# Optimization experiments

Measured on AMD Instinct MI355X. Metric: run time of the kernel, lower is better.

The kernel has to match this reference:

```python
import jax, jax.numpy as jnp
import numpy as np

B, TQ, TK, E, H, DH = 4, 1024, 1024, 1024, 16, 64
EPS = 1e-5

def setup_inputs() -> dict:
    key = jax.random.key(0)
    ks = jax.random.split(key, 16)
    s = 0.02
    return {
        "x": jax.random.normal(ks[0], (B, TQ, E), jnp.float32),
        "encoder_out": jax.random.normal(ks[1], (B, TK, E), jnp.float32),
        "Q1w": jax.random.normal(ks[2], (H, DH, E), jnp.float32) * s,
        "Q1b": jax.random.normal(ks[3], (H, DH), jnp.float32) * s,
        "Q2w": jax.random.normal(ks[4], (H, DH, E), jnp.float32) * s,
        "Q2b": jax.random.normal(ks[5], (H, DH), jnp.float32) * s,
        "K1w": jax.random.normal(ks[6], (H, DH, E), jnp.float32) * s,
        "K1b": jax.random.normal(ks[7], (H, DH), jnp.float32) * s,
        "K2w": jax.random.normal(ks[8], (H, DH, E), jnp.float32) * s,
        "K2b": jax.random.normal(ks[9], (H, DH), jnp.float32) * s,
        "Vw": jax.random.normal(ks[10], (H, DH, E), jnp.float32) * s,
        "Vb": jax.random.normal(ks[11], (H, DH), jnp.float32) * s,
        "lam": jax.random.uniform(ks[12], (H,), jnp.float32, 0.5, 1.0),
        "gn_gamma": jnp.ones((H * DH,), jnp.float32),
        "gn_beta": jnp.zeros((H * DH,), jnp.float32),
        "out_w": jax.random.normal(ks[13], (E, H * DH), jnp.float32) * s,
        "out_b": jax.random.normal(ks[14], (E,), jnp.float32) * s,
    }

def _proj(inp, w, b):
    # inp: [B,T,E], w: [H,DH,E] -> [B,H,T,DH]
    return jnp.einsum('bte,hde->bhtd', inp, w) + b[None, :, None, :]

def reference(x, encoder_out, Q1w, Q1b, Q2w, Q2b, K1w, K1b, K2w, K2b, Vw, Vb,
              lam, gn_gamma, gn_beta, out_w, out_b):
    scale = 1.0 / jnp.sqrt(jnp.float32(DH))
    q1 = _proj(x, Q1w, Q1b)
    q2 = _proj(x, Q2w, Q2b)
    k1 = _proj(encoder_out, K1w, K1b)
    k2 = _proj(encoder_out, K2w, K2b)
    v = _proj(encoder_out, Vw, Vb)
    s1 = jnp.einsum('bhtd,bhsd->bhts', q1, k1) * scale  # [B,H,TQ,TK]
    s2 = jnp.einsum('bhtd,bhsd->bhts', q2, k2) * scale
    w = jax.nn.softmax(s1, axis=-1) - lam[None, :, None, None] * jax.nn.softmax(s2, axis=-1)
    out = jnp.einsum('bhts,bhsd->bhtd', w, v)  # [B,H,TQ,DH]
    # GroupNorm(num_groups=H, channels=H*DH) over [B,C,T]: per (B,H) stats over (T,DH)
    mu = jnp.mean(out, axis=(2, 3), keepdims=True)
    var = jnp.mean(jnp.square(out - mu), axis=(2, 3), keepdims=True)
    normed = (out - mu) * jax.lax.rsqrt(var + EPS)
    g = gn_gamma.reshape(H, DH)[None, :, None, :]
    b_ = gn_beta.reshape(H, DH)[None, :, None, :]
    normed = normed * g + b_
    y = normed.transpose(0, 2, 1, 3).reshape(B, TQ, H * DH)
    return y @ out_w.T + out_b
```

## Files before the change

kernel.cpp:

```cpp
#include <hip/hip_runtime.h>
#include <cmath>

typedef __bf16 bf16_t;
typedef bf16_t bf16x8 __attribute__((ext_vector_type(8)));
typedef bf16_t bf16x4 __attribute__((ext_vector_type(4)));
typedef float  f32x4  __attribute__((ext_vector_type(4)));

#define Bn  4
#define TQn 1024
#define TKn 1024
#define En  1024
#define Hn  16
#define DHn 64

static constexpr float EPSv = 1e-5f;
static constexpr float C_SCALE = 0.18033688011112042f;

#define GLDS16(g, l)                                                         \
    __builtin_amdgcn_global_load_lds(                                        \
        (const __attribute__((address_space(1))) void*)(g),                  \
        (__attribute__((address_space(3))) void*)(l), 16, 0, 0)

__global__ __launch_bounds__(256)
void cvt_all(const float* __restrict__ x, const float* __restrict__ enc,
             const float* __restrict__ q1w, const float* __restrict__ q2w,
             const float* __restrict__ k1w, const float* __restrict__ k2w,
             const float* __restrict__ vw,  const float* __restrict__ outw,
             bf16_t* __restrict__ xb, bf16_t* __restrict__ encb,
             bf16_t* __restrict__ wq, bf16_t* __restrict__ wkv,
             bf16_t* __restrict__ wob)
{
    int idx = blockIdx.x * 256 + threadIdx.x;
    const float* src; bf16_t* dst;
    if      (idx < 1048576) { src = x    + (size_t)idx * 4;              dst = xb   + (size_t)idx * 4; }
    else if (idx < 2097152) { src = enc  + (size_t)(idx - 1048576) * 4;  dst = encb + (size_t)(idx - 1048576) * 4; }
    else if (idx < 2359296) { src = q1w  + (size_t)(idx - 2097152) * 4;  dst = wq   + (size_t)(idx - 2097152) * 4; }
    else if (idx < 2621440) { src = q2w  + (size_t)(idx - 2359296) * 4;  dst = wq   + 1048576 + (size_t)(idx - 2359296) * 4; }
    else if (idx < 2883584) { src = k1w  + (size_t)(idx - 2621440) * 4;  dst = wkv  + (size_t)(idx - 2621440) * 4; }
    else if (idx < 3145728) { src = k2w  + (size_t)(idx - 2883584) * 4;  dst = wkv  + 1048576 + (size_t)(idx - 2883584) * 4; }
    else if (idx < 3407872) { src = vw   + (size_t)(idx - 3145728) * 4;  dst = wkv  + 2097152 + (size_t)(idx - 3145728) * 4; }
    else                    { src = outw + (size_t)(idx - 3407872) * 4;  dst = wob  + (size_t)(idx - 3407872) * 4; }
    float4 v = *(const float4*)src;
    bf16x4 o;
    o[0] = (bf16_t)v.x; o[1] = (bf16_t)v.y; o[2] = (bf16_t)v.z; o[3] = (bf16_t)v.w;
    *(bf16x4*)dst = o;
}

__global__ __launch_bounds__(256, 3)
void gemm_proj(const bf16_t* __restrict__ xb, const bf16_t* __restrict__ encb,
               const bf16_t* __restrict__ wq, const bf16_t* __restrict__ wkv,
               const float* __restrict__ q1b, const float* __restrict__ q2b,
               const float* __restrict__ k1b, const float* __restrict__ k2b,
               const float* __restrict__ vb,
               bf16_t* __restrict__ q12, bf16_t* __restrict__ k12v)
{
    __shared__ bf16_t sA[128 * 64];
    __shared__ bf16_t sB[128 * 64];
    int bx = blockIdx.x;
    const bf16_t* A; const bf16_t* W; bf16_t* C; const float* bp; int blockN;
    if (bx < 16) {
        A = xb; W = wq; C = q12; blockN = bx << 7;
        bp = (blockN >> 10) ? q2b : q1b;
    } else {
        bx -= 16;
        A = encb; W = wkv; C = k12v; blockN = bx << 7;
        const int seg = blockN >> 10;
        bp = (seg == 0) ? k1b : ((seg == 1) ? k2b : vb);
    }
    const int blockM = blockIdx.y << 7;

    const int tid = threadIdx.x;
    const int w = tid >> 6, lane = tid & 63;
    const int q = lane >> 4, r = lane & 15;
    const int wm = w & 1, wn = w >> 1;

    f32x4 acc[4][4];
#pragma unroll
    for (int i = 0; i < 4; ++i)
#pragma unroll
        for (int j = 0; j < 4; ++j) acc[i][j] = (f32x4){0.f, 0.f, 0.f, 0.f};

    for (int k0 = 0; k0 < 1024; k0 += 64) {
#pragma unroll
        for (int c = 0; c < 4; ++c) {
            const int s = c * 256 + tid;
            const int row = s >> 3;
            const int cg = (s & 7) ^ (row & 7);
            GLDS16(A + (size_t)(blockM + row) * 1024 + k0 + cg * 8, sA + c * 2048 + w * 512);
            GLDS16(W + (size_t)(blockN + row) * 1024 + k0 + cg * 8, sB + c * 2048 + w * 512);
        }
        __syncthreads();
#pragma unroll
        for (int ks = 0; ks < 2; ++ks) {
            bf16x8 a[4], b[4];
#pragma unroll
            for (int i = 0; i < 4; ++i) {
                const int row = wm * 64 + i * 16 + r;
                const int g = (ks * 4 + q) ^ (row & 7);
                a[i] = *(const bf16x8*)&sA[row * 64 + g * 8];
            }
#pragma unroll
            for (int j = 0; j < 4; ++j) {
                const int row = wn * 64 + j * 16 + r;
                const int g = (ks * 4 + q) ^ (row & 7);
                b[j] = *(const bf16x8*)&sB[row * 64 + g * 8];
            }
#pragma unroll
            for (int i = 0; i < 4; ++i)
#pragma unroll
                for (int j = 0; j < 4; ++j)
                    acc[i][j] = __builtin_amdgcn_mfma_f32_16x16x32_bf16(a[i], b[j], acc[i][j], 0, 0, 0);
        }
        __syncthreads();
    }

    const int seg = blockN >> 10;
#pragma unroll
    for (int j = 0; j < 4; ++j) {
        const int n = blockN + wn * 64 + j * 16 + r;
        const float bv = bp[n & 1023];
#pragma unroll
        for (int i = 0; i < 4; ++i) {
            f32x4 v = acc[i][j];
#pragma unroll
            for (int e = 0; e < 4; ++e) {
                const int m = blockM + wm * 64 + i * 16 + q * 4 + e;
                const float val = v[e] + bv;
                const int bb = m >> 10, t = m & 1023;
                const int h = (n >> 6) & 15, d = n & 63;
                ((bf16_t*)C)[((((size_t)seg * 4 + bb) * 16 + h) * 1024 + t) * 64 + d] = (bf16_t)val;
            }
        }
    }
}

__global__ __launch_bounds__(256, 4)
void gemm_out(const bf16_t* __restrict__ yb, const bf16_t* __restrict__ wob,
              const float* __restrict__ outb, float* __restrict__ out)
{
    __shared__ bf16_t sA[64 * 64];
    __shared__ bf16_t sB[128 * 64];
    const int L = blockIdx.x;
    const int xcd = L & 7, kk = L >> 3;
    const int blockM = (xcd * 8 + (kk >> 3)) * 64;
    const int blockN = (kk & 7) * 128;

    const int tid = threadIdx.x;
    const int w = tid >> 6, lane = tid & 63;
    const int q = lane >> 4, r = lane & 15;

    f32x4 acc[4][2];
#pragma unroll
    for (int i = 0; i < 4; ++i)
#pragma unroll
        for (int j = 0; j < 2; ++j) acc[i][j] = (f32x4){0.f, 0.f, 0.f, 0.f};

    for (int k0 = 0; k0 < 1024; k0 += 64) {
#pragma unroll
        for (int c = 0; c < 2; ++c) {
            const int s = c * 256 + tid;
            const int row = s >> 3;
            const int cg = (s & 7) ^ (row & 7);
            GLDS16(yb + (size_t)(blockM + row) * 1024 + k0 + cg * 8, sA + c * 2048 + w * 512);
        }
#pragma unroll
        for (int c = 0; c < 4; ++c) {
            const int s = c * 256 + tid;
            const int row = s >> 3;
            const int cg = (s & 7) ^ (row & 7);
            GLDS16(wob + (size_t)(blockN + row) * 1024 + k0 + cg * 8, sB + c * 2048 + w * 512);
        }
        __syncthreads();
#pragma unroll
        for (int ks = 0; ks < 2; ++ks) {
            bf16x8 a[4], b[2];
#pragma unroll
            for (int i = 0; i < 4; ++i) {
                const int row = i * 16 + r;
                const int g = (ks * 4 + q) ^ (row & 7);
                a[i] = *(const bf16x8*)&sA[row * 64 + g * 8];
            }
#pragma unroll
            for (int j = 0; j < 2; ++j) {
                const int row = w * 32 + j * 16 + r;
                const int g = (ks * 4 + q) ^ (row & 7);
                b[j] = *(const bf16x8*)&sB[row * 64 + g * 8];
            }
#pragma unroll
            for (int i = 0; i < 4; ++i)
#pragma unroll
                for (int j = 0; j < 2; ++j)
                    acc[i][j] = __builtin_amdgcn_mfma_f32_16x16x32_bf16(a[i], b[j], acc[i][j], 0, 0, 0);
        }
        __syncthreads();
    }

#pragma unroll
    for (int j = 0; j < 2; ++j) {
        const int n = blockN + w * 32 + j * 16 + r;
        const float bv = outb[n];
#pragma unroll
        for (int i = 0; i < 4; ++i) {
            f32x4 v = acc[i][j];
#pragma unroll
            for (int e = 0; e < 4; ++e) {
                const int m = blockM + i * 16 + q * 4 + e;
                out[(size_t)m * 1024 + n] = v[e] + bv;
            }
        }
    }
}

__device__ __forceinline__ void compute_S(const bf16_t* __restrict__ sK,
                                          const bf16x8 (&fQ)[2],
                                          f32x4 (&S)[4], int q, int r)
{
#pragma unroll
    for (int i = 0; i < 4; ++i) S[i] = (f32x4){0.f, 0.f, 0.f, 0.f};
#pragma unroll
    for (int ks = 0; ks < 2; ++ks) {
        bf16x8 fK[4];
#pragma unroll
        for (int i = 0; i < 4; ++i) {
            const int row = i * 16 + r;
            const int g = (ks * 4 + q) ^ (row & 7);
            fK[i] = *(const bf16x8*)&sK[row * 64 + g * 8];
        }
        __builtin_amdgcn_s_setprio(1);
#pragma unroll
        for (int i = 0; i < 4; ++i)
            S[i] = __builtin_amdgcn_mfma_f32_16x16x32_bf16(fK[i], fQ[ks], S[i], 0, 0, 0);
        __builtin_amdgcn_s_setprio(0);
    }
}

__device__ __forceinline__ void softmax_pw(f32x4 (&S)[4], bf16_t* __restrict__ sPt,
                                           float& l, int w, int q, int r)
{
    const int t = w * 16 + r;
    float part = 0.f;
#pragma unroll
    for (int i = 0; i < 4; ++i) {
        bf16x4 pk;
#pragma unroll
        for (int e = 0; e < 4; ++e) {
            const float p = __builtin_amdgcn_exp2f(S[i][e] * C_SCALE);
            part += p;
            pk[e] = (bf16_t)p;
        }
        const int sb = i * 16 + q * 4;
        const int g = (sb >> 3) ^ (t & 7);
        *(bf16x4*)&sPt[t * 64 + g * 8 + (sb & 7)] = pk;
    }
    l += part;
}

__device__ __forceinline__ void pv(const bf16_t* __restrict__ sPt,
                                   const bf16x8 (&fV)[4][2],
                                   f32x4 (&O)[4], int w, int q, int r)
{
#pragma unroll
    for (int ks = 0; ks < 2; ++ks) {
        const int m = w * 16 + r;
        const int g = (ks * 4 + q) ^ (m & 7);
        bf16x8 fP = *(const bf16x8*)&sPt[m * 64 + g * 8];
        __builtin_amdgcn_s_setprio(1);
#pragma unroll
        for (int j = 0; j < 4; ++j)
            O[j] = __builtin_amdgcn_mfma_f32_16x16x32_bf16(fP, fV[j][ks], O[j], 0, 0, 0);
        __builtin_amdgcn_s_setprio(0);
    }
}

__global__ __launch_bounds__(512, 2)
void diff_attn_mfma(const bf16_t* __restrict__ q12, const bf16_t* __restrict__ k12v,
                    const float* __restrict__ lam, bf16_t* __restrict__ out,
                    float* __restrict__ stats)
{
    __shared__ bf16_t sK1[2][64 * 64];
    __shared__ bf16_t sK2[2][64 * 64];
    __shared__ bf16_t sVt[64 * 64];
    __shared__ bf16_t sPt[128 * 64];
    __shared__ float  sl1[128], sl2[128];
    __shared__ float  sred[16];

    const int tid = threadIdx.x;
    const int w = tid >> 6, lane = tid & 63;
    const int q = lane >> 4, r = lane & 15;
    const int bh = blockIdx.x, qt = blockIdx.y;
    const float lamv = lam[bh & (Hn - 1)];

    const size_t HT = (size_t)TKn * DHn;
    const bf16_t* q1g = q12 + (size_t)bh * HT + (size_t)qt * 128 * DHn;
    const bf16_t* q2g = q1g + 64 * HT;
    const bf16_t* k1g = k12v + (size_t)bh * HT;
    const bf16_t* k2g = k1g + 64 * HT;
    const bf16_t* vg  = k1g + 128 * HT;

    bf16x8 fQ1[2], fQ2[2];
    {
        const int t = w * 16 + r;
#pragma unroll
        for (int ks = 0; ks < 2; ++ks) {
            fQ1[ks] = *(const bf16x8*)(q1g + (size_t)t * 64 + ks * 32 + q * 8);
            fQ2[ks] = *(const bf16x8*)(q2g + (size_t)t * 64 + ks * 32 + q * 8);
        }
    }

    f32x4 O1[4], O2[4];
    float l1 = 0.f, l2 = 0.f;
#pragma unroll
    for (int j = 0; j < 4; ++j) { O1[j] = (f32x4){0.f,0.f,0.f,0.f}; O2[j] = (f32x4){0.f,0.f,0.f,0.f}; }

    {
        const int row = tid >> 3;
        const int cg = (tid & 7) ^ (row & 7);
        GLDS16(k1g + row * 64 + cg * 8, &sK1[0][tid * 8]);
        GLDS16(k2g + row * 64 + cg * 8, &sK2[0][tid * 8]);
        const int s = tid & 63;
        bf16x8 v0 = *(const bf16x8*)(vg + (size_t)s * 64 + w * 8);
#pragma unroll
        for (int i = 0; i < 8; ++i) {
            const int d = w * 8 + i;
            sVt[d * 64 + (((s >> 3) ^ i) << 3) + (s & 7)] = v0[i];
        }
        __syncthreads();
    }

    bf16x8 vr;
    for (int st = 0; st < TKn / 64; ++st) {
        const int cur = st & 1;
        if (st < 15) {
            const int row = tid >> 3;
            const int cg = (tid & 7) ^ (row & 7);
            GLDS16(k1g + (size_t)(st + 1) * 4096 + row * 64 + cg * 8, &sK1[cur ^ 1][tid * 8]);
            GLDS16(k2g + (size_t)(st + 1) * 4096 + row * 64 + cg * 8, &sK2[cur ^ 1][tid * 8]);
            vr = *(const bf16x8*)(vg + (size_t)(st + 1) * 4096 + (size_t)(tid & 63) * 64 + w * 8);
        }

        bf16x8 fV[4][2];
#pragma unroll
        for (int j = 0; j < 4; ++j)
#pragma unroll
            for (int ks = 0; ks < 2; ++ks) {
                const int d = j * 16 + r;
                const int g = (ks * 4 + q) ^ (d & 7);
                fV[j][ks] = *(const bf16x8*)&sVt[d * 64 + g * 8];
            }
        {
            f32x4 S[4];
            compute_S(sK1[cur], fQ1, S, q, r);
            softmax_pw(S, sPt, l1, w, q, r);
            pv(sPt, fV, O1, w, q, r);
        }
        {
            f32x4 S[4];
            compute_S(sK2[cur], fQ2, S, q, r);
            softmax_pw(S, sPt, l2, w, q, r);
            pv(sPt, fV, O2, w, q, r);
        }

        __syncthreads();
        if (st < 15) {
            const int s = tid & 63;
#pragma unroll
            for (int i = 0; i < 8; ++i) {
                const int d = w * 8 + i;
                sVt[d * 64 + (((s >> 3) ^ i) << 3) + (s & 7)] = vr[i];
            }
            __syncthreads();
        }
    }

    {
        float v1 = l1;
        v1 += __shfl_xor(v1, 16); v1 += __shfl_xor(v1, 32);
        float v2 = l2;
        v2 += __shfl_xor(v2, 16); v2 += __shfl_xor(v2, 32);
        if (q == 0) { sl1[w * 16 + r] = v1; sl2[w * 16 + r] = v2; }
    }

    bf16_t* op = out + ((size_t)bh * TQn + (size_t)qt * 128) * DHn;
    float ssum = 0.f, ssq = 0.f;
#pragma unroll
    for (int e = 0; e < 4; ++e) {
        const int t = w * 16 + q * 4 + e;
        const float inv1 = 1.0f / sl1[t];
        const float inv2 = lamv / sl2[t];
#pragma unroll
        for (int j = 0; j < 4; ++j) {
            const float o = O1[j][e] * inv1 - O2[j][e] * inv2;
            op[(size_t)t * 64 + j * 16 + r] = (bf16_t)o;
            ssum += o;
            ssq += o * o;
        }
    }
#pragma unroll
    for (int d = 1; d < 64; d <<= 1) {
        ssum += __shfl_xor(ssum, d);
        ssq  += __shfl_xor(ssq, d);
    }
    if (lane == 0) { sred[w] = ssum; sred[8 + w] = ssq; }
    __syncthreads();
    if (tid == 0) {
        float a = 0.f, b = 0.f;
#pragma unroll
        for (int k = 0; k < 8; ++k) { a += sred[k]; b += sred[8 + k]; }
        stats[(bh << 3) + qt]       = a;
        stats[512 + (bh << 3) + qt] = b;
    }
}

__global__ __launch_bounds__(256)
void gn_apply(const bf16_t* __restrict__ attn, const float* __restrict__ stats,
              const float* __restrict__ gamma, const float* __restrict__ beta,
              bf16_t* __restrict__ y)
{
    const int f = blockIdx.x * 256 + threadIdx.x;
    const int d8 = (f & 7) << 3;
    const int t  = (f >> 3) & 1023;
    const int bh = f >> 13;
    const int h  = bh & 15;
    const int b  = bh >> 4;
    const float* p1 = stats + (bh << 3);
    const float* p2 = stats + 512 + (bh << 3);
    float s1 = 0.f, s2 = 0.f;
#pragma unroll
    for (int k = 0; k < 8; ++k) { s1 += p1[k]; s2 += p2[k]; }
    const float mu = s1 * (1.f / 65536.f);
    const float var = s2 * (1.f / 65536.f) - mu * mu;
    const float rstd = rsqrtf(var + EPSv);
    bf16x8 v = *(const bf16x8*)&attn[((size_t)bh << 16) + t * 64 + d8];
    const int c = h * 64 + d8;
    const float* gp = gamma + c;
    const float* bp = beta + c;
    bf16x8 o;
#pragma unroll
    for (int i = 0; i < 8; ++i)
        o[i] = (bf16_t)(((float)v[i] - mu) * rstd * gp[i] + bp[i]);
    *(bf16x8*)&y[((size_t)(b * 1024 + t)) * 1024 + c] = o;
}

extern "C" void kernel_launch(void* const* d_in, const int* in_sizes, int n_in,
                              void* d_out, int out_size, void* d_ws, size_t ws_size,
                              hipStream_t stream)
{
    const float* x    = (const float*)d_in[0];
    const float* enc  = (const float*)d_in[1];
    const float* Q1w  = (const float*)d_in[2];
    const float* Q1b  = (const float*)d_in[3];
    const float* Q2w  = (const float*)d_in[4];
    const float* Q2b  = (const float*)d_in[5];
    const float* K1w  = (const float*)d_in[6];
    const float* K1b  = (const float*)d_in[7];
    const float* K2w  = (const float*)d_in[8];
    const float* K2b  = (const float*)d_in[9];
    const float* Vw   = (const float*)d_in[10];
    const float* Vb   = (const float*)d_in[11];
    const float* lam  = (const float*)d_in[12];
    const float* gng  = (const float*)d_in[13];
    const float* gnb  = (const float*)d_in[14];
    const float* outw = (const float*)d_in[15];
    const float* outb = (const float*)d_in[16];
    float* out = (float*)d_out;

    bf16_t* xb   = (bf16_t*)d_ws;
    bf16_t* encb = xb   + 4194304;
    bf16_t* wq   = encb + 4194304;
    bf16_t* wkv  = wq   + 2097152;
    bf16_t* wob  = wkv  + 3145728;
    bf16_t* q12  = wob  + 1048576;
    bf16_t* k12v = q12  + 8388608;
    bf16_t* attnb= xb;
    bf16_t* yb   = encb;
    float*  stats= (float*)wq;

    cvt_all<<<14336, 256, 0, stream>>>(x, enc, Q1w, Q2w, K1w, K2w, Vw, outw,
                                       xb, encb, wq, wkv, wob);

    gemm_proj<<<dim3(40, 32), 256, 0, stream>>>(xb, encb, wq, wkv,
                                                Q1b, Q2b, K1b, K2b, Vb, q12, k12v);

    diff_attn_mfma<<<dim3(64, 8), 512, 0, stream>>>(q12, k12v, lam, attnb, stats);

    gn_apply<<<2048, 256, 0, stream>>>(attnb, stats, gng, gnb, yb);

    gemm_out<<<512, 256, 0, stream>>>(yb, wob, outb, out);
}
```

Before: 251.2 us.

## Rewrite differential attention with 32x32 MFMA, register P, and split-stream waves

The attention kernel is rebuilt around 32x32x16 MFMA tiles. Each half of the block's waves now handles one softmax stream (q1/k1 or q2/k2), and the probabilities are packed to bf16 in registers using cvt_pk and permlane32_swap instead of round-tripping through shared memory. Results from the two streams are combined through an LDS exchange at the end. Separately, the projection GEMM epilogue stages its output tile in LDS so it can write 16-byte vector rows instead of scattered bf16 stores. The changes target LDS traffic and uncoalesced stores, at the cost of an extra block barrier and a larger occupancy request (launch bounds 512,4).

Result: no change. 249.4 us (-0.7%).

```diff
diff --git a/kernel.cpp b/kernel.cpp
--- a/kernel.cpp
+++ b/kernel.cpp
@@ -5,6 +5,8 @@
 typedef bf16_t bf16x8 __attribute__((ext_vector_type(8)));
 typedef bf16_t bf16x4 __attribute__((ext_vector_type(4)));
 typedef float  f32x4  __attribute__((ext_vector_type(4)));
+typedef float  f32x16 __attribute__((ext_vector_type(16)));
+typedef unsigned int u32x4v __attribute__((ext_vector_type(4)));
 
 #define Bn  4
 #define TQn 1024
@@ -54,9 +56,13 @@
                const float* __restrict__ vb,
                bf16_t* __restrict__ q12, bf16_t* __restrict__ k12v)
 {
-    __shared__ bf16_t sA[128 * 64];
-    __shared__ bf16_t sB[128 * 64];
+    __shared__ __align__(16) bf16_t sAB[2][128 * 64];
+    bf16_t* const sA = &sAB[0][0];
+    bf16_t* const sB = &sAB[1][0];
+    bf16_t* const sC = &sAB[0][0];
+
     int bx = blockIdx.x;
+    const int blockM = blockIdx.y << 7;
     const bf16_t* A; const bf16_t* W; bf16_t* C; const float* bp; int blockN;
     if (bx < 16) {
         A = xb; W = wq; C = q12; blockN = bx << 7;
@@ -64,10 +70,9 @@
     } else {
         bx -= 16;
         A = encb; W = wkv; C = k12v; blockN = bx << 7;
-        const int seg = blockN >> 10;
-        bp = (seg == 0) ? k1b : ((seg == 1) ? k2b : vb);
-    }
-    const int blockM = blockIdx.y << 7;
+        const int seg0 = blockN >> 10;
+        bp = (seg0 == 0) ? k1b : ((seg0 == 1) ? k2b : vb);
+    }
 
     const int tid = threadIdx.x;
     const int w = tid >> 6, lane = tid & 63;
@@ -114,23 +119,32 @@
         __syncthreads();
     }
 
-    const int seg = blockN >> 10;
 #pragma unroll
     for (int j = 0; j < 4; ++j) {
-        const int n = blockN + wn * 64 + j * 16 + r;
-        const float bv = bp[n & 1023];
+        const int n = wn * 64 + j * 16 + r;
+        const float bv = bp[(blockN + n) & 1023];
 #pragma unroll
         for (int i = 0; i < 4; ++i) {
             f32x4 v = acc[i][j];
 #pragma unroll
             for (int e = 0; e < 4; ++e) {
-                const int m = blockM + wm * 64 + i * 16 + q * 4 + e;
-                const float val = v[e] + bv;
-                const int bb = m >> 10, t = m & 1023;
-                const int h = (n >> 6) & 15, d = n & 63;
-                ((bf16_t*)C)[((((size_t)seg * 4 + bb) * 16 + h) * 1024 + t) * 64 + d] = (bf16_t)val;
-            }
-        }
+                const int m = wm * 64 + i * 16 + q * 4 + e;
+                sC[m * 128 + (((n >> 3) ^ (m & 7)) << 3) + (n & 7)] = (bf16_t)(v[e] + bv);
+            }
+        }
+    }
+    __syncthreads();
+    const int seg = blockN >> 10;
+#pragma unroll
+    for (int v8 = 0; v8 < 8; ++v8) {
+        const int flat = v8 * 256 + tid;
+        const int m = flat >> 4;
+        const int nb = flat & 15;
+        bf16x8 row = *(const bf16x8*)&sC[m * 128 + ((nb ^ (m & 7)) << 3)];
+        const int gm = blockM + m, gn = blockN + nb * 8;
+        const int bb = gm >> 10, t = gm & 1023;
+        const int h = (gn >> 6) & 15, d = gn & 63;
+        *(bf16x8*)&C[((((size_t)seg * 4 + bb) * 16 + h) * 1024 + t) * 64 + d] = row;
     }
 }
 
@@ -211,114 +225,72 @@
     }
 }
 
-__device__ __forceinline__ void compute_S(const bf16_t* __restrict__ sK,
-                                          const bf16x8 (&fQ)[2],
-                                          f32x4 (&S)[4], int q, int r)
-{
-#pragma unroll
-    for (int i = 0; i < 4; ++i) S[i] = (f32x4){0.f, 0.f, 0.f, 0.f};
-#pragma unroll
-    for (int ks = 0; ks < 2; ++ks) {
-        bf16x8 fK[4];
-#pragma unroll
-        for (int i = 0; i < 4; ++i) {
-            const int row = i * 16 + r;
-            const int g = (ks * 4 + q) ^ (row & 7);
-            fK[i] = *(const bf16x8*)&sK[row * 64 + g * 8];
-        }
-        __builtin_amdgcn_s_setprio(1);
-#pragma unroll
-        for (int i = 0; i < 4; ++i)
-            S[i] = __builtin_amdgcn_mfma_f32_16x16x32_bf16(fK[i], fQ[ks], S[i], 0, 0, 0);
-        __builtin_amdgcn_s_setprio(0);
-    }
-}
-
-__device__ __forceinline__ void softmax_pw(f32x4 (&S)[4], bf16_t* __restrict__ sPt,
-                                           float& l, int w, int q, int r)
-{
-    const int t = w * 16 + r;
-    float part = 0.f;
-#pragma unroll
-    for (int i = 0; i < 4; ++i) {
-        bf16x4 pk;
-#pragma unroll
-        for (int e = 0; e < 4; ++e) {
-            const float p = __builtin_amdgcn_exp2f(S[i][e] * C_SCALE);
-            part += p;
-            pk[e] = (bf16_t)p;
-        }
-        const int sb = i * 16 + q * 4;
-        const int g = (sb >> 3) ^ (t & 7);
-        *(bf16x4*)&sPt[t * 64 + g * 8 + (sb & 7)] = pk;
-    }
-    l += part;
-}
-
-__device__ __forceinline__ void pv(const bf16_t* __restrict__ sPt,
-                                   const bf16x8 (&fV)[4][2],
-                                   f32x4 (&O)[4], int w, int q, int r)
-{
-#pragma unroll
-    for (int ks = 0; ks < 2; ++ks) {
-        const int m = w * 16 + r;
-        const int g = (ks * 4 + q) ^ (m & 7);
-        bf16x8 fP = *(const bf16x8*)&sPt[m * 64 + g * 8];
-        __builtin_amdgcn_s_setprio(1);
-#pragma unroll
-        for (int j = 0; j < 4; ++j)
-            O[j] = __builtin_amdgcn_mfma_f32_16x16x32_bf16(fP, fV[j][ks], O[j], 0, 0, 0);
-        __builtin_amdgcn_s_setprio(0);
-    }
-}
-
-__global__ __launch_bounds__(512, 2)
-void diff_attn_mfma(const bf16_t* __restrict__ q12, const bf16_t* __restrict__ k12v,
-                    const float* __restrict__ lam, bf16_t* __restrict__ out,
-                    float* __restrict__ stats)
-{
-    __shared__ bf16_t sK1[2][64 * 64];
-    __shared__ bf16_t sK2[2][64 * 64];
-    __shared__ bf16_t sVt[64 * 64];
-    __shared__ bf16_t sPt[128 * 64];
-    __shared__ float  sl1[128], sl2[128];
-    __shared__ float  sred[16];
+__device__ __forceinline__ unsigned cvtpk_bf16(float a, float b)
+{
+    unsigned r;
+    asm("v_cvt_pk_bf16_f32 %0, %1, %2" : "=v"(r) : "v"(a), "v"(b));
+    return r;
+}
+
+__device__ __forceinline__ void pack_pa(const f32x16& p, bf16x8& pa0, bf16x8& pa1)
+{
+    unsigned a0 = cvtpk_bf16(p[0], p[1]),   b0 = cvtpk_bf16(p[4], p[5]);
+    asm("v_permlane32_swap_b32 %0, %1" : "+v"(a0), "+v"(b0));
+    unsigned a1 = cvtpk_bf16(p[2], p[3]),   b1 = cvtpk_bf16(p[6], p[7]);
+    asm("v_permlane32_swap_b32 %0, %1" : "+v"(a1), "+v"(b1));
+    pa0 = __builtin_bit_cast(bf16x8, (u32x4v){a0, a1, b0, b1});
+    unsigned a2 = cvtpk_bf16(p[8], p[9]),   b2 = cvtpk_bf16(p[12], p[13]);
+    asm("v_permlane32_swap_b32 %0, %1" : "+v"(a2), "+v"(b2));
+    unsigned a3 = cvtpk_bf16(p[10], p[11]), b3 = cvtpk_bf16(p[14], p[15]);
+    asm("v_permlane32_swap_b32 %0, %1" : "+v"(a3), "+v"(b3));
+    pa1 = __builtin_bit_cast(bf16x8, (u32x4v){a2, a3, b2, b3});
+}
+
+__global__ __launch_bounds__(512, 4)
+void diff_attn32(const bf16_t* __restrict__ q12, const bf16_t* __restrict__ k12v,
+                 const float* __restrict__ lam, bf16_t* __restrict__ out,
+                 float* __restrict__ stats)
+{
+    __shared__ __align__(16) bf16_t arena[20480];
+    bf16_t* const sK1 = arena;
+    bf16_t* const sK2 = arena + 8192;
+    bf16_t* const sVt = arena + 16384;
+    float*  const xchg = (float*)arena;
+    __shared__ float sl[2][128];
+    __shared__ float sred[16];
 
     const int tid = threadIdx.x;
     const int w = tid >> 6, lane = tid & 63;
-    const int q = lane >> 4, r = lane & 15;
+    const int st_id = w >> 2, wv = w & 3;
+    const int hi = lane >> 5, lo = lane & 31;
     const int bh = blockIdx.x, qt = blockIdx.y;
     const float lamv = lam[bh & (Hn - 1)];
 
     const size_t HT = (size_t)TKn * DHn;
-    const bf16_t* q1g = q12 + (size_t)bh * HT + (size_t)qt * 128 * DHn;
-    const bf16_t* q2g = q1g + 64 * HT;
+    const bf16_t* qg  = q12 + (size_t)(st_id * 64 + bh) * HT + (size_t)qt * 128 * DHn;
     const bf16_t* k1g = k12v + (size_t)bh * HT;
     const bf16_t* k2g = k1g + 64 * HT;
     const bf16_t* vg  = k1g + 128 * HT;
-
-    bf16x8 fQ1[2], fQ2[2];
-    {
-        const int t = w * 16 + r;
-#pragma unroll
-        for (int ks = 0; ks < 2; ++ks) {
-            fQ1[ks] = *(const bf16x8*)(q1g + (size_t)t * 64 + ks * 32 + q * 8);
-            fQ2[ks] = *(const bf16x8*)(q2g + (size_t)t * 64 + ks * 32 + q * 8);
-        }
-    }
-
-    f32x4 O1[4], O2[4];
-    float l1 = 0.f, l2 = 0.f;
-#pragma unroll
-    for (int j = 0; j < 4; ++j) { O1[j] = (f32x4){0.f,0.f,0.f,0.f}; O2[j] = (f32x4){0.f,0.f,0.f,0.f}; }
+    const bf16_t* const sKs = st_id ? sK2 : sK1;
+
+    bf16x8 fQ[4];
+#pragma unroll
+    for (int dk = 0; dk < 4; ++dk)
+        fQ[dk] = *(const bf16x8*)(qg + (size_t)(wv * 32 + lo) * 64 + dk * 16 + hi * 8);
+
+    f32x16 O0, O1;
+#pragma unroll
+    for (int e = 0; e < 16; ++e) { O0[e] = 0.f; O1[e] = 0.f; }
+    float lsum = 0.f;
 
     {
         const int row = tid >> 3;
         const int cg = (tid & 7) ^ (row & 7);
-        GLDS16(k1g + row * 64 + cg * 8, &sK1[0][tid * 8]);
-        GLDS16(k2g + row * 64 + cg * 8, &sK2[0][tid * 8]);
+        GLDS16(k1g + row * 64 + cg * 8, sK1 + tid * 8);
+        GLDS16(k2g + row * 64 + cg * 8, sK2 + tid * 8);
         const int s = tid & 63;
         bf16x8 v0 = *(const bf16x8*)(vg + (size_t)s * 64 + w * 8);
+        __syncthreads();
 #pragma unroll
         for (int i = 0; i < 8; ++i) {
             const int d = w * 8 + i;
@@ -333,31 +305,43 @@
         if (st < 15) {
             const int row = tid >> 3;
             const int cg = (tid & 7) ^ (row & 7);
-            GLDS16(k1g + (size_t)(st + 1) * 4096 + row * 64 + cg * 8, &sK1[cur ^ 1][tid * 8]);
-            GLDS16(k2g + (size_t)(st + 1) * 4096 + row * 64 + cg * 8, &sK2[cur ^ 1][tid * 8]);
+            GLDS16(k1g + (size_t)(st + 1) * 4096 + row * 64 + cg * 8, sK1 + (cur ^ 1) * 4096 + tid * 8);
+            GLDS16(k2g + (size_t)(st + 1) * 4096 + row * 64 + cg * 8, sK2 + (cur ^ 1) * 4096 + tid * 8);
             vr = *(const bf16x8*)(vg + (size_t)(st + 1) * 4096 + (size_t)(tid & 63) * 64 + w * 8);
         }
 
-        bf16x8 fV[4][2];
-#pragma unroll
-        for (int j = 0; j < 4; ++j)
-#pragma unroll
-            for (int ks = 0; ks < 2; ++ks) {
-                const int d = j * 16 + r;
-                const int g = (ks * 4 + q) ^ (d & 7);
-                fV[j][ks] = *(const bf16x8*)&sVt[d * 64 + g * 8];
-            }
-        {
-            f32x4 S[4];
-            compute_S(sK1[cur], fQ1, S, q, r);
-            softmax_pw(S, sPt, l1, w, q, r);
-            pv(sPt, fV, O1, w, q, r);
-        }
-        {
-            f32x4 S[4];
-            compute_S(sK2[cur], fQ2, S, q, r);
-            softmax_pw(S, sPt, l2, w, q, r);
-            pv(sPt, fV, O2, w, q, r);
+        const bf16_t* sKc = sKs + cur * 4096;
+#pragma unroll
+        for (int kb = 0; kb < 2; ++kb) {
+            f32x16 S;
+#pragma unroll
+            for (int e = 0; e < 16; ++e) S[e] = 0.f;
+            __builtin_amdgcn_s_setprio(1);
+#pragma unroll
+            for (int dk = 0; dk < 4; ++dk) {
+                bf16x8 fk = *(const bf16x8*)&sKc[(kb * 32 + lo) * 64 + (((dk * 2 + hi) ^ (lo & 7)) << 3)];
+                S = __builtin_amdgcn_mfma_f32_32x32x16_bf16(fk, fQ[dk], S, 0, 0, 0);
+            }
+            __builtin_amdgcn_s_setprio(0);
+#pragma unroll
+            for (int e = 0; e < 16; ++e) {
+                S[e] = __builtin_amdgcn_exp2f(S[e] * C_SCALE);
+                lsum += S[e];
+            }
+            bf16x8 pa0, pa1;
+            pack_pa(S, pa0, pa1);
+            const int c0 = ((kb * 4 + 0 * 2 + hi) ^ (lo & 7)) << 3;
+            const int c1 = ((kb * 4 + 1 * 2 + hi) ^ (lo & 7)) << 3;
+            bf16x8 fv00 = *(const bf16x8*)&sVt[(0 * 32 + lo) * 64 + c0];
+            bf16x8 fv01 = *(const bf16x8*)&sVt[(0 * 32 + lo) * 64 + c1];
+            bf16x8 fv10 = *(const bf16x8*)&sVt[(1 * 32 + lo) * 64 + c0];
+            bf16x8 fv11 = *(const bf16x8*)&sVt[(1 * 32 + lo) * 64 + c1];
+            __builtin_amdgcn_s_setprio(1);
+            O0 = __builtin_amdgcn_mfma_f32_32x32x16_bf16(pa0, fv00, O0, 0, 0, 0);
+            O0 = __builtin_amdgcn_mfma_f32_32x32x16_bf16(pa1, fv01, O0, 0, 0, 0);
+            O1 = __builtin_amdgcn_mfma_f32_32x32x16_bf16(pa0, fv10, O1, 0, 0, 0);
+            O1 = __builtin_amdgcn_mfma_f32_32x32x16_bf16(pa1, fv11, O1, 0, 0, 0);
+            __builtin_amdgcn_s_setprio(0);
         }
 
         __syncthreads();
@@ -372,42 +356,45 @@
         }
     }
 
-    {
-        float v1 = l1;
-        v1 += __shfl_xor(v1, 16); v1 += __shfl_xor(v1, 32);
-        float v2 = l2;
-        v2 += __shfl_xor(v2, 16); v2 += __shfl_xor(v2, 32);
-        if (q == 0) { sl1[w * 16 + r] = v1; sl2[w * 16 + r] = v2; }
-    }
-
-    bf16_t* op = out + ((size_t)bh * TQn + (size_t)qt * 128) * DHn;
-    float ssum = 0.f, ssq = 0.f;
-#pragma unroll
-    for (int e = 0; e < 4; ++e) {
-        const int t = w * 16 + q * 4 + e;
-        const float inv1 = 1.0f / sl1[t];
-        const float inv2 = lamv / sl2[t];
-#pragma unroll
-        for (int j = 0; j < 4; ++j) {
-            const float o = O1[j][e] * inv1 - O2[j][e] * inv2;
-            op[(size_t)t * 64 + j * 16 + r] = (bf16_t)o;
-            ssum += o;
-            ssq += o * o;
-        }
-    }
-#pragma unroll
-    for (int d = 1; d < 64; d <<= 1) {
-        ssum += __shfl_xor(ssum, d);
-        ssq  += __shfl_xor(ssq, d);
-    }
-    if (lane == 0) { sred[w] = ssum; sred[8 + w] = ssq; }
+    lsum += __shfl_xor(lsum, 32);
+    if (hi == 0) sl[st_id][wv * 32 + lo] = lsum;
+
+    if (st_id == 1) {
+#pragma unroll
+        for (int reg = 0; reg < 16; ++reg) {
+            const int t = wv * 32 + (reg & 3) + 8 * (reg >> 2) + 4 * hi;
+            const float inv2 = lamv / sl[1][t];
+            xchg[t * 64 + lo]      = O0[reg] * inv2;
+            xchg[t * 64 + 32 + lo] = O1[reg] * inv2;
+        }
+    }
+    __syncthreads();
+
+    if (st_id == 0) {
+        float ssum = 0.f, ssq = 0.f;
+        bf16_t* op = out + ((size_t)bh * TQn + (size_t)qt * 128) * DHn;
+#pragma unroll
+        for (int reg = 0; reg < 16; ++reg) {
+            const int t = wv * 32 + (reg & 3) + 8 * (reg >> 2) + 4 * hi;
+            const float inv1 = 1.0f / sl[0][t];
+            const float o0 = O0[reg] * inv1 - xchg[t * 64 + lo];
+            const float o1 = O1[reg] * inv1 - xchg[t * 64 + 32 + lo];
+            op[(size_t)t * 64 + lo]      = (bf16_t)o0;
+            op[(size_t)t * 64 + 32 + lo] = (bf16_t)o1;
+            ssum += o0 + o1;
+            ssq  += o0 * o0 + o1 * o1;
+        }
+#pragma unroll
+        for (int d = 1; d < 64; d <<= 1) {
+            ssum += __shfl_xor(ssum, d);
+            ssq  += __shfl_xor(ssq, d);
+        }
+        if (lane == 0) { sred[wv] = ssum; sred[8 + wv] = ssq; }
+    }
     __syncthreads();
     if (tid == 0) {
-        float a = 0.f, b = 0.f;
-#pragma unroll
-        for (int k = 0; k < 8; ++k) { a += sred[k]; b += sred[8 + k]; }
-        stats[(bh << 3) + qt]       = a;
-        stats[512 + (bh << 3) + qt] = b;
+        stats[(bh << 3) + qt]       = sred[0] + sred[1] + sred[2] + sred[3];
+        stats[512 + (bh << 3) + qt] = sred[8] + sred[9] + sred[10] + sred[11];
     }
 }
 
@@ -481,7 +468,7 @@
     gemm_proj<<<dim3(40, 32), 256, 0, stream>>>(xb, encb, wq, wkv,
                                                 Q1b, Q2b, K1b, K2b, Vb, q12, k12v);
 
-    diff_attn_mfma<<<dim3(64, 8), 512, 0, stream>>>(q12, k12v, lam, attnb, stats);
+    diff_attn32<<<dim3(64, 8), 512, 0, stream>>>(q12, k12v, lam, attnb, stats);
 
     gn_apply<<<2048, 256, 0, stream>>>(attnb, stats, gng, gnb, yb);
 
```
